# Performance work log

Measured on AMD Instinct MI355X. Metric: run time of the kernel, lower is better.

The kernel has to match this reference:

```python
import jax, jax.numpy as jnp
import numpy as np

B, D, S, F, C, H, OUT = 4, 60, 512, 158, 64, 128, 1
LN_EPS = 1e-5


def setup_inputs() -> dict:
    key = jax.random.key(0)
    ks = jax.random.split(key, 12)
    g = lambda k, shape, s=0.05: jax.random.normal(k, shape, dtype=jnp.float32) * s
    return dict(
        x=jax.random.normal(ks[0], (B, D, S, F), dtype=jnp.float32),
        feature_mask=jax.random.randint(ks[1], (B, D, S), 0, 2).astype(bool),
        wq=g(ks[2], (F, C)), bq=jnp.zeros((C,), jnp.float32),
        wk=g(ks[3], (F, C)), bk=jnp.zeros((C,), jnp.float32),
        wv=g(ks[4], (F, C)), bv=jnp.zeros((C,), jnp.float32),
        ln_g=jnp.ones((F + C,), jnp.float32), ln_b=jnp.zeros((F + C,), jnp.float32),
        w_ih=g(ks[5], (3 * H, F + C)), w_hh=g(ks[6], (3 * H, H)),
        b_ih=jnp.zeros((3 * H,), jnp.float32), b_hh=jnp.zeros((3 * H,), jnp.float32),
        w1=g(ks[7], (H, H // 2)), b1=jnp.zeros((H // 2,), jnp.float32),
        w2=g(ks[8], (H // 2, OUT)), b2=jnp.zeros((OUT,), jnp.float32),
    )


def reference(x, feature_mask, wq, bq, wk, bk, wv, bv, ln_g, ln_b,
              w_ih, w_hh, b_ih, b_hh, w1, b1, w2, b2):
    b, d, s, f = x.shape
    c = wq.shape[1]
    h_dim = w_hh.shape[1]

    # --- market context attention, vectorized over (batch, days) ---
    Q = x @ wq + bq            # (B,D,S,C)
    K = x @ wk + bk
    V = x @ wv + bv
    scores = jnp.einsum('bdsc,bdtc->bdst', Q, K) / jnp.sqrt(jnp.float32(c))
    scores = jnp.where(feature_mask[:, :, None, :], scores, -1e9)  # mask keys
    attn = jax.nn.softmax(scores, axis=-1)
    ctx = jnp.einsum('bdst,bdtc->bdsc', attn, V)       # (B,D,S,C)
    ctx = jnp.where(feature_mask[..., None], ctx, 0.0)  # mask queries
    denom = jnp.maximum(feature_mask.sum(axis=2), 1).astype(x.dtype)  # (B,D)
    market = ctx.sum(axis=2) / denom[..., None]         # (B,D,C)

    # --- concat + layernorm ---
    aug = jnp.concatenate(
        [x, jnp.broadcast_to(market[:, :, None, :], (b, d, s, c))], axis=-1)
    mu = aug.mean(-1, keepdims=True)
    var = aug.var(-1, keepdims=True)
    aug = (aug - mu) / jnp.sqrt(var + LN_EPS) * ln_g + ln_b  # (B,D,S,F+C)

    # --- GRU over days, batch = B*S independent sequences ---
    seq = aug.transpose(1, 0, 2, 3).reshape(d, b * s, f + c)  # (D, N, F+C)
    x_proj = seq @ w_ih.T + b_ih                               # (D, N, 3H)

    def step(h, xp):
        hp = h @ w_hh.T + b_hh
        xr, xz, xn = jnp.split(xp, 3, axis=-1)
        hr, hz, hn = jnp.split(hp, 3, axis=-1)
        r = jax.nn.sigmoid(xr + hr)
        z = jax.nn.sigmoid(xz + hz)
        n = jnp.tanh(xn + r * hn)
        return (1.0 - z) * n + z * h, None

    h0 = jnp.zeros((b * s, h_dim), x.dtype)
    h_last, _ = jax.lax.scan(step, h0, x_proj)  # last-step output
    h_last = h_last.reshape(b, s, h_dim)

    # --- output head (dropout inactive in eval) ---
    hid = jax.nn.relu(h_last @ w1 + b1)
    return hid @ w2 + b2  # (B, S, OUT)
```

## Files before the change

### kernel.cpp

```cpp
#include <hip/hip_runtime.h>
#include <hip/hip_bf16.h>
#include <math.h>

#define BB 4
#define DD 60
#define SS 512
#define FF 158
#define CC 64
#define HH 128
#define FC 222
#define G3 384
#define NN 2048
#define BDN 240

typedef _Float16 f16x8 __attribute__((ext_vector_type(8)));
typedef float f32x4 __attribute__((ext_vector_type(4)));

__device__ __forceinline__ float sigmoidf_(float x){ return 1.0f/(1.0f+__expf(-x)); }
__device__ __forceinline__ float tanhf_(float x){
    float e = __expf(-2.0f*fabsf(x));
    float t = (1.0f - e)/(1.0f + e);
    return copysignf(t, x);
}

__global__ void prep_kernel(const float* __restrict__ w_ih,
                            const float* __restrict__ wq, const float* __restrict__ wk,
                            const float* __restrict__ wv, const float* __restrict__ w_hh,
                            _Float16* __restrict__ wf16, _Float16* __restrict__ wqkv,
                            _Float16* __restrict__ whh16){
    int idx = blockIdx.x*256 + threadIdx.x;
    if (idx < 384*224){
        int n = idx / 224, k = idx % 224;
        wf16[idx] = (k < FC) ? (_Float16)w_ih[n*FC + k] : (_Float16)0.0f;
    } else if (idx < 384*224 + 192*160){
        int i2 = idx - 384*224;
        int n = i2 / 160, k = i2 % 160;
        float v = 0.0f;
        if (k < FF){
            if (n < 64)       v = wq[k*CC + n];
            else if (n < 128) v = wk[k*CC + (n-64)];
            else              v = wv[k*CC + (n-128)];
        }
        wqkv[i2] = (_Float16)v;
    } else {
        int i3 = idx - (384*224 + 192*160);
        if (i3 < 384*128)
            whh16[i3] = (_Float16)w_hh[i3];
    }
}

__global__ __launch_bounds__(256) void qkv_kernel(const float* __restrict__ x,
                           const _Float16* __restrict__ wqkv,
                           const float* __restrict__ bq, const float* __restrict__ bk,
                           const float* __restrict__ bv,
                           _Float16* __restrict__ Qh, _Float16* __restrict__ Kh,
                           float* __restrict__ V){
    __shared__ _Float16 xa[5][64][40];
    int tid  = threadIdx.x;
    int lane = tid & 63, wv = tid >> 6;
    int col  = lane & 15, quad = lane >> 4;
    int row0 = blockIdx.x * 64;

    f16x8 bfr[3][5];
    #pragma unroll
    for (int nt = 0; nt < 3; ++nt){
        int n = wv*48 + nt*16 + col;
        #pragma unroll
        for (int kq = 0; kq < 5; ++kq)
            bfr[nt][kq] = *(const f16x8*)&wqkv[n*160 + kq*32 + quad*8];
    }

    for (int i = tid; i < 64*160; i += 256){
        int r = i / 160, k = i % 160;
        float v = (k < FF) ? x[(size_t)(row0 + r)*FF + k] : 0.0f;
        xa[k >> 5][r][k & 31] = (_Float16)v;
    }
    __syncthreads();

    float bias[3];
    #pragma unroll
    for (int nt = 0; nt < 3; ++nt){
        int n = wv*48 + nt*16 + col;
        bias[nt] = (n < 64) ? bq[n] : (n < 128 ? bk[n-64] : bv[n-128]);
    }

    #pragma unroll 1
    for (int mt = 0; mt < 4; ++mt){
        f16x8 a[5];
        #pragma unroll
        for (int kq = 0; kq < 5; ++kq)
            a[kq] = *(const f16x8*)&xa[kq][mt*16 + col][quad*8];
        #pragma unroll
        for (int nt = 0; nt < 3; ++nt){
            f32x4 c = {0.0f, 0.0f, 0.0f, 0.0f};
            #pragma unroll
            for (int kq = 0; kq < 5; ++kq)
                c = __builtin_amdgcn_mfma_f32_16x16x32_f16(a[kq], bfr[nt][kq], c, 0, 0, 0);
            int n = wv*48 + nt*16 + col;
            #pragma unroll
            for (int reg = 0; reg < 4; ++reg){
                int row = row0 + mt*16 + quad*4 + reg;
                float val = c[reg] + bias[nt];
                if (n < 64)       Qh[(size_t)row*CC + n]       = (_Float16)val;
                else if (n < 128) Kh[(size_t)row*CC + (n-64)]  = (_Float16)val;
                else              V [(size_t)row*CC + (n-128)] = val;
            }
        }
    }
}

__global__ __launch_bounds__(512) void attn_kernel(const _Float16* __restrict__ Qh,
                                                   const _Float16* __restrict__ Kh,
                                                   const int* __restrict__ mask,
                                                   const float* __restrict__ V,
                                                   float* __restrict__ market){
    __shared__ _Float16 kf[2][512][32];
    __shared__ float w_sh[512];
    __shared__ float mk_lds[512];

    int tid  = threadIdx.x;
    int bd   = blockIdx.x;
    int lane = tid & 63, wv = tid >> 6;
    int col  = lane & 15, quad = lane >> 4;

    const _Float16* qb = Qh + (size_t)(bd*SS)*CC;
    const _Float16* kb = Kh + (size_t)(bd*SS)*CC;

    {
        int t = tid;
        w_sh[t] = 0.0f;
        mk_lds[t] = (mask[bd*SS + t] != 0) ? 1.0f : 0.0f;
    }
    for (int i = tid; i < 4096; i += 512){
        int t = i >> 3, ch = i & 7;
        *(f16x8*)&kf[ch >> 2][t][(ch & 3)*8] = *(const f16x8*)&kb[t*CC + ch*8];
    }

    f16x8 a0[4], a1[4];
    #pragma unroll
    for (int af = 0; af < 4; ++af){
        int row = wv*64 + af*16 + col;
        a0[af] = *(const f16x8*)&qb[row*CC + quad*8];
        a1[af] = *(const f16x8*)&qb[row*CC + 32 + quad*8];
    }
    __syncthreads();

    float lacc[4][4] = {{0,0,0,0},{0,0,0,0},{0,0,0,0},{0,0,0,0}};
    #pragma unroll 2
    for (int kt = 0; kt < 32; ++kt){
        f16x8 b0 = *(const f16x8*)&kf[0][kt*16 + col][quad*8];
        f16x8 b1 = *(const f16x8*)&kf[1][kt*16 + col][quad*8];
        float mkv = mk_lds[kt*16 + col];
        #pragma unroll
        for (int af = 0; af < 4; ++af){
            f32x4 c = {0.0f, 0.0f, 0.0f, 0.0f};
            c = __builtin_amdgcn_mfma_f32_16x16x32_f16(a0[af], b0, c, 0, 0, 0);
            c = __builtin_amdgcn_mfma_f32_16x16x32_f16(a1[af], b1, c, 0, 0, 0);
            #pragma unroll
            for (int reg = 0; reg < 4; ++reg)
                lacc[af][reg] += __expf(c[reg]*0.125f) * mkv;
        }
    }
    float crv[4][4];
    #pragma unroll
    for (int af = 0; af < 4; ++af){
        #pragma unroll
        for (int reg = 0; reg < 4; ++reg){
            float l = lacc[af][reg];
            l += __shfl_xor(l, 1, 64);
            l += __shfl_xor(l, 2, 64);
            l += __shfl_xor(l, 4, 64);
            l += __shfl_xor(l, 8, 64);
            int row = wv*64 + af*16 + quad*4 + reg;
            crv[af][reg] = mk_lds[row] / l;
        }
    }

    #pragma unroll 2
    for (int kt = 0; kt < 32; ++kt){
        f16x8 b0 = *(const f16x8*)&kf[0][kt*16 + col][quad*8];
        f16x8 b1 = *(const f16x8*)&kf[1][kt*16 + col][quad*8];
        float s = 0.0f;
        #pragma unroll
        for (int af = 0; af < 4; ++af){
            f32x4 c = {0.0f, 0.0f, 0.0f, 0.0f};
            c = __builtin_amdgcn_mfma_f32_16x16x32_f16(a0[af], b0, c, 0, 0, 0);
            c = __builtin_amdgcn_mfma_f32_16x16x32_f16(a1[af], b1, c, 0, 0, 0);
            #pragma unroll
            for (int reg = 0; reg < 4; ++reg)
                s = fmaf(__expf(c[reg]*0.125f), crv[af][reg], s);
        }
        s += __shfl_xor(s, 16, 64);
        s += __shfl_xor(s, 32, 64);
        if (quad == 0)
            atomicAdd(&w_sh[kt*16 + col], s);
    }
    __syncthreads();

    float* msum = (float*)kf;
    {
        int c = tid & 63, grp = tid >> 6;
        const float* vb = V + (size_t)(bd*SS)*CC;
        float acc = 0.0f;
        int t0 = grp*64;
        #pragma unroll 4
        for (int t = t0; t < t0 + 64; ++t)
            acc = fmaf(w_sh[t]*mk_lds[t], vb[(size_t)t*CC + c], acc);
        msum[grp*64 + c] = acc;
    }
    __syncthreads();
    if (tid < 64){
        float s = 0.0f;
        #pragma unroll
        for (int g = 0; g < 8; ++g) s += msum[g*64 + tid];
        float cnt = 0.0f;
        #pragma unroll
        for (int j = 0; j < 8; ++j) cnt += mk_lds[tid + 64*j];
        #pragma unroll
        for (int o = 1; o < 64; o <<= 1) cnt += __shfl_xor(cnt, o, 64);
        market[bd*CC + tid] = s / fmaxf(cnt, 1.0f);
    }
}

__global__ __launch_bounds__(512, 2) void xproj_kernel(const float* __restrict__ x,
                             const float* __restrict__ market,
                             const float* __restrict__ ln_g, const float* __restrict__ ln_b,
                             const _Float16* __restrict__ wf16, const float* __restrict__ b_ih,
                             _Float16* __restrict__ XP){
    __shared__ _Float16 aug[7][64][32];
    int tid  = threadIdx.x;
    int lane = tid & 63, wv = tid >> 6;
    int col  = lane & 15, quad = lane >> 4;
    int row0 = blockIdx.x * 64;

    f16x8 bfr[3][7];
    #pragma unroll
    for (int nt = 0; nt < 3; ++nt){
        int n = wv*48 + nt*16 + col;
        #pragma unroll
        for (int kq = 0; kq < 7; ++kq)
            bfr[nt][kq] = *(const f16x8*)&wf16[n*224 + kq*32 + quad*8];
    }

    {
        int wrow = wv*8 + (lane >> 3);
        int g    = lane & 7;
        int row  = row0 + wrow;
        int d = row / NN, n = row % NN;
        int b = n >> 9, s = n & 511;
        const float* xr = &x[((size_t)((b*DD + d)*SS) + s)*FF];
        const float* mr = &market[(b*DD + d)*CC];
        float v[28];
        float sum = 0.0f, sq = 0.0f;
        #pragma unroll
        for (int j = 0; j < 28; ++j){
            int f = g + 8*j;
            float vv = 0.0f;
            if (f < FF) vv = xr[f];
            else if (f < FC) vv = mr[f - FF];
            v[j] = vv;
            sum += vv; sq += vv*vv;
        }
        sum += __shfl_xor(sum,1,64); sq += __shfl_xor(sq,1,64);
        sum += __shfl_xor(sum,2,64); sq += __shfl_xor(sq,2,64);
        sum += __shfl_xor(sum,4,64); sq += __shfl_xor(sq,4,64);
        float mu   = sum * (1.0f/222.0f);
        float var  = sq * (1.0f/222.0f) - mu*mu;
        float rstd = rsqrtf(var + 1e-5f);
        #pragma unroll
        for (int j = 0; j < 28; ++j){
            int f = g + 8*j;
            float val = (f < FC) ? ((v[j]-mu)*rstd*ln_g[f] + ln_b[f]) : 0.0f;
            aug[f>>5][wrow][f&31] = (_Float16)val;
        }
    }
    __syncthreads();

    float bias[3];
    #pragma unroll
    for (int nt = 0; nt < 3; ++nt) bias[nt] = b_ih[wv*48 + nt*16 + col];
    #pragma unroll 1
    for (int mt = 0; mt < 4; ++mt){
        f16x8 a[7];
        #pragma unroll
        for (int kq = 0; kq < 7; ++kq)
            a[kq] = *(const f16x8*)&aug[kq][mt*16 + col][quad*8];
        #pragma unroll
        for (int nt = 0; nt < 3; ++nt){
            f32x4 c = {0.0f, 0.0f, 0.0f, 0.0f};
            #pragma unroll
            for (int kq = 0; kq < 7; ++kq)
                c = __builtin_amdgcn_mfma_f32_16x16x32_f16(a[kq], bfr[nt][kq], c, 0, 0, 0);
            int nn = wv*48 + nt*16 + col;
            #pragma unroll
            for (int reg = 0; reg < 4; ++reg){
                int m = quad*4 + reg;
                XP[(size_t)(row0 + mt*16 + m)*G3 + nn] = (_Float16)(c[reg] + bias[nt]);
            }
        }
    }
}

__global__ __launch_bounds__(256, 2) void gru_kernel(const _Float16* __restrict__ XP,
                                                     const _Float16* __restrict__ whh16,
                                                     const float* __restrict__ b_hh,
                                                     const float* __restrict__ w1, const float* __restrict__ b1,
                                                     const float* __restrict__ w2, const float* __restrict__ b2,
                                                     float* __restrict__ out){
    __shared__ _Float16 hfrag[2][4][16][32];
    __shared__ float hp_sh[4][3][4][32];
    __shared__ float h_f32[4][132];

    int tid  = threadIdx.x;
    int lane = tid & 63, wv = tid >> 6;
    int col  = lane & 15, quad = lane >> 4;
    int row0 = blockIdx.x * 4;

    for (int i = tid; i < 2*4*16*32; i += 256) ((_Float16*)hfrag)[i] = (_Float16)0.0f;

    f16x8 bfr[3][2][4];
    #pragma unroll
    for (int g = 0; g < 3; ++g){
        #pragma unroll
        for (int hf = 0; hf < 2; ++hf){
            int n = g*128 + wv*32 + hf*16 + col;
            #pragma unroll
            for (int kq = 0; kq < 4; ++kq)
                bfr[g][hf][kq] = *(const f16x8*)&whh16[(size_t)n*HH + kq*32 + quad*8];
        }
    }

    int u  = lane & 31;
    int cc = wv*32 + u;
    int sb = lane >> 5;
    float bh0 = b_hh[cc], bh1 = b_hh[128 + cc], bh2 = b_hh[256 + cc];

    float hcur[2] = {0.0f, 0.0f};

    const _Float16* xbase0 = XP + (size_t)(row0 + sb)*G3 + cc;
    const _Float16* xbase1 = XP + (size_t)(row0 + 2 + sb)*G3 + cc;
    const size_t DSTRIDE = (size_t)NN*G3;

    float xb[10][2][3];
    #pragma unroll
    for (int cs = 0; cs < 10; ++cs){
        const _Float16* b0 = xbase0 + (size_t)cs*DSTRIDE;
        const _Float16* b1 = xbase1 + (size_t)cs*DSTRIDE;
        xb[cs][0][0] = (float)b0[0]; xb[cs][0][1] = (float)b0[128]; xb[cs][0][2] = (float)b0[256];
        xb[cs][1][0] = (float)b1[0]; xb[cs][1][1] = (float)b1[128]; xb[cs][1][2] = (float)b1[256];
    }
    __syncthreads();

    #pragma unroll 1
    for (int chunk = 0; chunk < 6; ++chunk){
        #pragma unroll
        for (int cs = 0; cs < 10; ++cs){
            int d = chunk*10 + cs;
            int p = d & 1;
            float xcur[2][3];
            #pragma unroll
            for (int j = 0; j < 2; ++j){
                xcur[j][0] = xb[cs][j][0];
                xcur[j][1] = xb[cs][j][1];
                xcur[j][2] = xb[cs][j][2];
            }
            if (cs == 9 && chunk < 5){
                size_t off = (size_t)(chunk + 1)*10*DSTRIDE;
                #pragma unroll
                for (int c2 = 0; c2 < 10; ++c2){
                    const _Float16* b0 = xbase0 + off + (size_t)c2*DSTRIDE;
                    const _Float16* b1 = xbase1 + off + (size_t)c2*DSTRIDE;
                    xb[c2][0][0] = (float)b0[0]; xb[c2][0][1] = (float)b0[128]; xb[c2][0][2] = (float)b0[256];
                    xb[c2][1][0] = (float)b1[0]; xb[c2][1][1] = (float)b1[128]; xb[c2][1][2] = (float)b1[256];
                }
            }
            f16x8 a[4];
            #pragma unroll
            for (int kq = 0; kq < 4; ++kq)
                a[kq] = *(const f16x8*)&hfrag[p][kq][col][quad*8];
            #pragma unroll
            for (int g = 0; g < 3; ++g){
                #pragma unroll
                for (int hf = 0; hf < 2; ++hf){
                    f32x4 c = {0.0f, 0.0f, 0.0f, 0.0f};
                    #pragma unroll
                    for (int kq = 0; kq < 4; ++kq)
                        c = __builtin_amdgcn_mfma_f32_16x16x32_f16(a[kq], bfr[g][hf][kq], c, 0, 0, 0);
                    if (quad == 0){
                        #pragma unroll
                        for (int reg = 0; reg < 4; ++reg)
                            hp_sh[wv][g][reg][hf*16 + col] = c[reg];
                    }
                }
            }
            #pragma unroll
            for (int j = 0; j < 2; ++j){
                int seq = j*2 + sb;
                float hr = hp_sh[wv][0][seq][u] + bh0;
                float hz = hp_sh[wv][1][seq][u] + bh1;
                float hn = hp_sh[wv][2][seq][u] + bh2;
                float r  = sigmoidf_(xcur[j][0] + hr);
                float z  = sigmoidf_(xcur[j][1] + hz);
                float n  = tanhf_(xcur[j][2] + r*hn);
                float hnew = (1.0f - z)*n + z*hcur[j];
                hcur[j] = hnew;
                hfrag[1 - p][wv][seq][u] = (_Float16)hnew;
            }
            __syncthreads();
        }
    }

    #pragma unroll
    for (int j = 0; j < 2; ++j){
        int seq = j*2 + sb;
        h_f32[seq][cc] = hcur[j];
    }
    __syncthreads();

    if (tid < 64){
        int c2 = tid;
        #pragma unroll 1
        for (int r = 0; r < 4; ++r){
            float a0 = 0.0f, a1 = 0.0f;
            #pragma unroll 8
            for (int k = 0; k < 64; ++k){
                a0 = fmaf(h_f32[r][k],      w1[k*64 + c2],        a0);
                a1 = fmaf(h_f32[r][64 + k], w1[(64 + k)*64 + c2], a1);
            }
            float hid = fmaxf(a0 + a1 + b1[c2], 0.0f);
            float o = hid * w2[c2];
            #pragma unroll
            for (int off = 1; off < 64; off <<= 1) o += __shfl_xor(o, off, 64);
            if (c2 == 0) out[row0 + r] = o + b2[0];
        }
    }
}

extern "C" void kernel_launch(void* const* d_in, const int* in_sizes, int n_in,
                              void* d_out, int out_size, void* d_ws, size_t ws_size,
                              hipStream_t stream) {
    const float* x    = (const float*)d_in[0];
    const int*   mask = (const int*)d_in[1];
    const float* wq   = (const float*)d_in[2];
    const float* bq   = (const float*)d_in[3];
    const float* wk   = (const float*)d_in[4];
    const float* bk   = (const float*)d_in[5];
    const float* wv   = (const float*)d_in[6];
    const float* bv   = (const float*)d_in[7];
    const float* ln_g = (const float*)d_in[8];
    const float* ln_b = (const float*)d_in[9];
    const float* w_ih = (const float*)d_in[10];
    const float* w_hh = (const float*)d_in[11];
    const float* b_ih = (const float*)d_in[12];
    const float* b_hh = (const float*)d_in[13];
    const float* w1   = (const float*)d_in[14];
    const float* b1   = (const float*)d_in[15];
    const float* w2   = (const float*)d_in[16];
    const float* b2   = (const float*)d_in[17];

    float* ws = (float*)d_ws;
    _Float16* Qh  = (_Float16*)ws;
    _Float16* Kh  = (_Float16*)(ws + 3932160);
    float*    V   = ws + 7864320;
    _Float16* XP  = (_Float16*)ws;
    float* market = ws + 23592960;
    _Float16* wf16 = (_Float16*)(ws + 23608320);
    _Float16* wqkv = (_Float16*)(ws + 23651328);
    _Float16* whh16= (_Float16*)(ws + 23666688);

    prep_kernel<<<648, 256, 0, stream>>>(w_ih, wq, wk, wv, w_hh, wf16, wqkv, whh16);
    qkv_kernel<<<1920, 256, 0, stream>>>(x, wqkv, bq, bk, bv, Qh, Kh, V);
    attn_kernel<<<240, 512, 0, stream>>>(Qh, Kh, mask, V, market);
    xproj_kernel<<<1920, 512, 0, stream>>>(x, market, ln_g, ln_b, wf16, b_ih, XP);
    gru_kernel<<<512, 256, 0, stream>>>(XP, whh16, b_hh, w1, b1, w2, b2, (float*)d_out);
}
```

Measured before the change: 369.5 us.

## Restructure GRU kernel: 16 sequences per block, gates computed in MFMA registers

Each GRU block now handles 16 sequences with 8 waves instead of 4 sequences with 4 waves, so the 16-row MFMA tile is fully used rather than mostly padding. Gate nonlinearities are applied directly on the MFMA accumulator registers, which removes the shared-memory staging of h·W_hh results. X-projection prefetch becomes a rolling three-buffer scheme one step ahead, and tanh uses a cheaper formula. The grid drops from 512 to 128 blocks, which may underfill the GPU's CUs and lengthen the serial 60-step chain for each block.

```diff
diff --git a/kernel.cpp b/kernel.cpp
--- a/kernel.cpp
+++ b/kernel.cpp
@@ -17,10 +17,9 @@
 typedef float f32x4 __attribute__((ext_vector_type(4)));
 
 __device__ __forceinline__ float sigmoidf_(float x){ return 1.0f/(1.0f+__expf(-x)); }
-__device__ __forceinline__ float tanhf_(float x){
-    float e = __expf(-2.0f*fabsf(x));
-    float t = (1.0f - e)/(1.0f + e);
-    return copysignf(t, x);
+__device__ __forceinline__ float tanh_fast_(float x){
+    float e = __expf(2.0f*x);
+    return 1.0f - 2.0f/(e + 1.0f);
 }
 
 __global__ void prep_kernel(const float* __restrict__ w_ih,
@@ -301,133 +300,102 @@
     }
 }
 
-__global__ __launch_bounds__(256, 2) void gru_kernel(const _Float16* __restrict__ XP,
-                                                     const _Float16* __restrict__ whh16,
-                                                     const float* __restrict__ b_hh,
-                                                     const float* __restrict__ w1, const float* __restrict__ b1,
-                                                     const float* __restrict__ w2, const float* __restrict__ b2,
-                                                     float* __restrict__ out){
+#define XLOAD(dst, base_) do{                                                   \
+    _Pragma("unroll") for (int rg_ = 0; rg_ < 4; ++rg_)                         \
+    _Pragma("unroll") for (int g_ = 0; g_ < 3; ++g_)                            \
+        dst[rg_][g_] = (base_)[rg_*G3 + g_*HH];                                 \
+}while(0)
+
+#define GRU_STEP(PRD, PWR, XC, XPF, DOPF) do{                                   \
+    if (DOPF) { XLOAD(XPF, xp_d + 2*DSTR); }                                    \
+    f16x8 a_[4];                                                                \
+    _Pragma("unroll") for (int kq = 0; kq < 4; ++kq)                            \
+        a_[kq] = *(const f16x8*)&hfrag[PRD][kq][col][quad*8];                   \
+    f32x4 c0 = {0,0,0,0}, c1 = {0,0,0,0}, c2 = {0,0,0,0};                       \
+    _Pragma("unroll") for (int kq = 0; kq < 4; ++kq)                            \
+        c0 = __builtin_amdgcn_mfma_f32_16x16x32_f16(a_[kq], bfr[0][kq], c0, 0,0,0); \
+    _Pragma("unroll") for (int kq = 0; kq < 4; ++kq)                            \
+        c1 = __builtin_amdgcn_mfma_f32_16x16x32_f16(a_[kq], bfr[1][kq], c1, 0,0,0); \
+    _Pragma("unroll") for (int kq = 0; kq < 4; ++kq)                            \
+        c2 = __builtin_amdgcn_mfma_f32_16x16x32_f16(a_[kq], bfr[2][kq], c2, 0,0,0); \
+    _Pragma("unroll") for (int rg = 0; rg < 4; ++rg){                           \
+        float r_ = sigmoidf_((float)XC[rg][0] + c0[rg] + bh0);                  \
+        float z_ = sigmoidf_((float)XC[rg][1] + c1[rg] + bh1);                  \
+        float n_ = tanh_fast_((float)XC[rg][2] + r_*(c2[rg] + bh2));            \
+        float h_ = n_ + z_*(hcur[rg] - n_);                                     \
+        hcur[rg] = h_;                                                          \
+        hfrag[PWR][w >> 1][quad*4 + rg][(w & 1)*16 + col] = (_Float16)h_;       \
+    }                                                                           \
+    xp_d += DSTR;                                                               \
+    __syncthreads();                                                            \
+}while(0)
+
+__global__ __launch_bounds__(512) void gru_kernel(const _Float16* __restrict__ XP,
+                                                  const _Float16* __restrict__ whh16,
+                                                  const float* __restrict__ b_hh,
+                                                  const float* __restrict__ w1, const float* __restrict__ b1,
+                                                  const float* __restrict__ w2, const float* __restrict__ b2,
+                                                  float* __restrict__ out){
     __shared__ _Float16 hfrag[2][4][16][32];
-    __shared__ float hp_sh[4][3][4][32];
-    __shared__ float h_f32[4][132];
-
-    int tid  = threadIdx.x;
-    int lane = tid & 63, wv = tid >> 6;
-    int col  = lane & 15, quad = lane >> 4;
-    int row0 = blockIdx.x * 4;
-
-    for (int i = tid; i < 2*4*16*32; i += 256) ((_Float16*)hfrag)[i] = (_Float16)0.0f;
-
-    f16x8 bfr[3][2][4];
+    __shared__ float h_sh[16][132];
+
+    const int tid  = threadIdx.x;
+    const int lane = tid & 63, w = tid >> 6;
+    const int col  = lane & 15, quad = lane >> 4;
+    const int row0 = blockIdx.x * 16;
+
+    for (int i = tid; i < 4*16*32; i += 512)
+        ((_Float16*)hfrag)[i] = (_Float16)0.0f;
+
+    f16x8 bfr[3][4];
     #pragma unroll
     for (int g = 0; g < 3; ++g){
         #pragma unroll
-        for (int hf = 0; hf < 2; ++hf){
-            int n = g*128 + wv*32 + hf*16 + col;
-            #pragma unroll
-            for (int kq = 0; kq < 4; ++kq)
-                bfr[g][hf][kq] = *(const f16x8*)&whh16[(size_t)n*HH + kq*32 + quad*8];
-        }
-    }
-
-    int u  = lane & 31;
-    int cc = wv*32 + u;
-    int sb = lane >> 5;
-    float bh0 = b_hh[cc], bh1 = b_hh[128 + cc], bh2 = b_hh[256 + cc];
-
-    float hcur[2] = {0.0f, 0.0f};
-
-    const _Float16* xbase0 = XP + (size_t)(row0 + sb)*G3 + cc;
-    const _Float16* xbase1 = XP + (size_t)(row0 + 2 + sb)*G3 + cc;
-    const size_t DSTRIDE = (size_t)NN*G3;
-
-    float xb[10][2][3];
-    #pragma unroll
-    for (int cs = 0; cs < 10; ++cs){
-        const _Float16* b0 = xbase0 + (size_t)cs*DSTRIDE;
-        const _Float16* b1 = xbase1 + (size_t)cs*DSTRIDE;
-        xb[cs][0][0] = (float)b0[0]; xb[cs][0][1] = (float)b0[128]; xb[cs][0][2] = (float)b0[256];
-        xb[cs][1][0] = (float)b1[0]; xb[cs][1][1] = (float)b1[128]; xb[cs][1][2] = (float)b1[256];
-    }
+        for (int kq = 0; kq < 4; ++kq)
+            bfr[g][kq] = *(const f16x8*)&whh16[(size_t)(g*HH + w*16 + col)*HH + kq*32 + quad*8];
+    }
+
+    const float bh0 = b_hh[0*HH + w*16 + col];
+    const float bh1 = b_hh[1*HH + w*16 + col];
+    const float bh2 = b_hh[2*HH + w*16 + col];
+
+    const size_t DSTR = (size_t)NN * G3;
+    const _Float16* xp_d = XP + (size_t)(row0 + quad*4)*G3 + (w*16 + col);
+
+    _Float16 xA[4][3], xB[4][3], xC[4][3];
+    XLOAD(xA, xp_d);
+    XLOAD(xB, xp_d + DSTR);
+
+    float hcur[4] = {0.0f, 0.0f, 0.0f, 0.0f};
     __syncthreads();
 
     #pragma unroll 1
-    for (int chunk = 0; chunk < 6; ++chunk){
-        #pragma unroll
-        for (int cs = 0; cs < 10; ++cs){
-            int d = chunk*10 + cs;
-            int p = d & 1;
-            float xcur[2][3];
-            #pragma unroll
-            for (int j = 0; j < 2; ++j){
-                xcur[j][0] = xb[cs][j][0];
-                xcur[j][1] = xb[cs][j][1];
-                xcur[j][2] = xb[cs][j][2];
-            }
-            if (cs == 9 && chunk < 5){
-                size_t off = (size_t)(chunk + 1)*10*DSTRIDE;
-                #pragma unroll
-                for (int c2 = 0; c2 < 10; ++c2){
-                    const _Float16* b0 = xbase0 + off + (size_t)c2*DSTRIDE;
-                    const _Float16* b1 = xbase1 + off + (size_t)c2*DSTRIDE;
-                    xb[c2][0][0] = (float)b0[0]; xb[c2][0][1] = (float)b0[128]; xb[c2][0][2] = (float)b0[256];
-                    xb[c2][1][0] = (float)b1[0]; xb[c2][1][1] = (float)b1[128]; xb[c2][1][2] = (float)b1[256];
-                }
-            }
-            f16x8 a[4];
-            #pragma unroll
-            for (int kq = 0; kq < 4; ++kq)
-                a[kq] = *(const f16x8*)&hfrag[p][kq][col][quad*8];
-            #pragma unroll
-            for (int g = 0; g < 3; ++g){
-                #pragma unroll
-                for (int hf = 0; hf < 2; ++hf){
-                    f32x4 c = {0.0f, 0.0f, 0.0f, 0.0f};
-                    #pragma unroll
-                    for (int kq = 0; kq < 4; ++kq)
-                        c = __builtin_amdgcn_mfma_f32_16x16x32_f16(a[kq], bfr[g][hf][kq], c, 0, 0, 0);
-                    if (quad == 0){
-                        #pragma unroll
-                        for (int reg = 0; reg < 4; ++reg)
-                            hp_sh[wv][g][reg][hf*16 + col] = c[reg];
-                    }
-                }
-            }
-            #pragma unroll
-            for (int j = 0; j < 2; ++j){
-                int seq = j*2 + sb;
-                float hr = hp_sh[wv][0][seq][u] + bh0;
-                float hz = hp_sh[wv][1][seq][u] + bh1;
-                float hn = hp_sh[wv][2][seq][u] + bh2;
-                float r  = sigmoidf_(xcur[j][0] + hr);
-                float z  = sigmoidf_(xcur[j][1] + hz);
-                float n  = tanhf_(xcur[j][2] + r*hn);
-                float hnew = (1.0f - z)*n + z*hcur[j];
-                hcur[j] = hnew;
-                hfrag[1 - p][wv][seq][u] = (_Float16)hnew;
-            }
-            __syncthreads();
-        }
-    }
-
-    #pragma unroll
-    for (int j = 0; j < 2; ++j){
-        int seq = j*2 + sb;
-        h_f32[seq][cc] = hcur[j];
-    }
-    __syncthreads();
-
-    if (tid < 64){
-        int c2 = tid;
-        #pragma unroll 1
-        for (int r = 0; r < 4; ++r){
-            float a0 = 0.0f, a1 = 0.0f;
+    for (int ch = 0; ch < 10; ++ch){
+        const int pf = (ch < 9);
+        GRU_STEP(0, 1, xA, xC, 1);
+        GRU_STEP(1, 0, xB, xA, 1);
+        GRU_STEP(0, 1, xC, xB, 1);
+        GRU_STEP(1, 0, xA, xC, 1);
+        GRU_STEP(0, 1, xB, xA, pf);
+        GRU_STEP(1, 0, xC, xB, pf);
+    }
+
+    #pragma unroll
+    for (int rg = 0; rg < 4; ++rg)
+        h_sh[quad*4 + rg][w*16 + col] = hcur[rg];
+    __syncthreads();
+
+    {
+        int c2 = tid & 63;
+        int rb = tid >> 6;
+        #pragma unroll
+        for (int rr = 0; rr < 2; ++rr){
+            int r = rb + rr*8;
+            float acc = 0.0f;
             #pragma unroll 8
-            for (int k = 0; k < 64; ++k){
-                a0 = fmaf(h_f32[r][k],      w1[k*64 + c2],        a0);
-                a1 = fmaf(h_f32[r][64 + k], w1[(64 + k)*64 + c2], a1);
-            }
-            float hid = fmaxf(a0 + a1 + b1[c2], 0.0f);
+            for (int k = 0; k < 128; ++k)
+                acc = fmaf(h_sh[r][k], w1[k*64 + c2], acc);
+            float hid = fmaxf(acc + b1[c2], 0.0f);
             float o = hid * w2[c2];
             #pragma unroll
             for (int off = 1; off < 64; off <<= 1) o += __shfl_xor(o, off, 64);
@@ -472,5 +440,5 @@
     qkv_kernel<<<1920, 256, 0, stream>>>(x, wqkv, bq, bk, bv, Qh, Kh, V);
     attn_kernel<<<240, 512, 0, stream>>>(Qh, Kh, mask, V, market);
     xproj_kernel<<<1920, 512, 0, stream>>>(x, market, ln_g, ln_b, wf16, b_ih, XP);
-    gru_kernel<<<512, 256, 0, stream>>>(XP, whh16, b_hh, w1, b1, w2, b2, (float*)d_out);
-}
+    gru_kernel<<<128, 512, 0, stream>>>(XP, whh16, b_hh, w1, b1, w2, b2, (float*)d_out);
+}
```

After: 371.8 us. Within noise of the previous version (+0.6%).
